# Kernel optimization log

Hardware: AMD Instinct MI355X
Metric: run time of the kernel (lower is better)

Reference implementation:

```python
import jax, jax.numpy as jnp
import numpy as np

NUM_HEADS = 16
BLOCK_SIZE = 64


def setup_inputs() -> dict:
    key = jax.random.key(0)
    ks = jax.random.split(key, 4)
    B, S, D = 4, 8192, 1024
    x = jax.random.normal(ks[0], (B, S, D), dtype=jnp.float32)
    Wq = jax.random.normal(ks[1], (D, D), dtype=jnp.float32) * 0.02
    Wk = jax.random.normal(ks[2], (D, D), dtype=jnp.float32) * 0.02
    Wv = jax.random.normal(ks[3], (D, D), dtype=jnp.float32) * 0.02
    bq = jnp.zeros((D,), dtype=jnp.float32)
    bk = jnp.zeros((D,), dtype=jnp.float32)
    bv = jnp.zeros((D,), dtype=jnp.float32)
    return {"x": x, "Wq": Wq, "bq": bq, "Wk": Wk, "bk": bk, "Wv": Wv, "bv": bv}


def reference(x, Wq, bq, Wk, bk, Wv, bv):
    # Block-diagonal local self-attention: token i attends only to tokens in
    # its own block [i//bs*bs, (i//bs+1)*bs). Equivalent to the original dense
    # mask, but computed block-wise (never materializing the SxS score matrix).
    B, S, D = x.shape
    H, bs = NUM_HEADS, BLOCK_SIZE
    d = D // H
    nb = S // bs

    q = (x @ Wq + bq).reshape(B, nb, bs, H, d)
    k = (x @ Wk + bk).reshape(B, nb, bs, H, d)
    v = (x @ Wv + bv).reshape(B, nb, bs, H, d)

    scale = 1.0 / jnp.sqrt(jnp.asarray(d, dtype=x.dtype))
    # per-block scores: [B, nb, H, bs, bs]
    scores = jnp.einsum("bnihd,bnjhd->bnhij", q, k) * scale
    attn = jax.nn.softmax(scores, axis=-1)
    out = jnp.einsum("bnhij,bnjhd->bnihd", attn, v)  # [B, nb, bs, H, d]
    return out.reshape(B, S, D)
```

## Files before the change

### kernel.cpp

```cpp
#include <hip/hip_runtime.h>
#include <hip/hip_bf16.h>

typedef __attribute__((ext_vector_type(8))) short short8;
typedef __attribute__((ext_vector_type(4))) float f32x4;
typedef unsigned short u16;

#define DIM     1024
#define NHEAD   16
#define HDIM    64
#define AS1 __attribute__((address_space(1)))
#define AS3 __attribute__((address_space(3)))

__device__ __forceinline__ u16 f2b(float f) {
  union { float f; unsigned u; } v; v.f = f;
  unsigned r = (v.u + 0x7FFFu + ((v.u >> 16) & 1u)) >> 16;
  return (u16)r;
}

__global__ void cvt_x_kernel(const float* __restrict__ in, u16* __restrict__ out, int n8) {
  int i = blockIdx.x * 256 + threadIdx.x;
  if (i >= n8) return;
  const float4* p = (const float4*)in + (size_t)i * 2;
  float4 a = p[0], c = p[1];
  short8 o;
  o[0] = (short)f2b(a.x); o[1] = (short)f2b(a.y); o[2] = (short)f2b(a.z); o[3] = (short)f2b(a.w);
  o[4] = (short)f2b(c.x); o[5] = (short)f2b(c.y); o[6] = (short)f2b(c.z); o[7] = (short)f2b(c.w);
  *((short8*)out + i) = o;
}

__global__ void cvt_wT_kernel(const float* __restrict__ Wq, const float* __restrict__ Wk,
                              const float* __restrict__ Wv, u16* __restrict__ wT) {
  int t = blockIdx.x * 256 + threadIdx.x;
  int mat = t >> 17;
  int rem = t & 131071;
  int kg  = rem >> 10;
  int n   = rem & 1023;
  const float* W = (mat == 0) ? Wq : (mat == 1) ? Wk : Wv;
  short8 v;
  #pragma unroll
  for (int i = 0; i < 8; ++i) v[i] = (short)f2b(W[(size_t)(kg * 8 + i) * DIM + n]);
  *(short8*)(wT + ((size_t)mat << 20) + (size_t)n * DIM + kg * 8) = v;
}

#define STAGE(matB, h, ktile) do { \
  const u16* _s = (matB) ? srcB : srcA; \
  _Pragma("unroll") \
  for (int _j = 0; _j < 2; ++_j) { \
    int _c = _j * 8 + wid; \
    __builtin_amdgcn_global_load_lds( \
      (const AS1 void*)(_s + (size_t)((h) * 128 + _c * 8) * DIM + (ktile) * 64), \
      (AS3 void*)(lds + ((((ktile) & 1) << 15) + ((matB) << 14) + ((h) << 13) + _c * 512)), \
      16, 0, 0); \
  } \
} while (0)

#define LDA(d, g) do { \
  _Pragma("unroll") \
  for (int _mi = 0; _mi < 4; ++_mi) { \
    int _r = abase + ((g) * 4 + _mi) * 1024 + ((d) << 15); \
    a[_mi * 2]     = *(const short8*)(lds + _r + sx0); \
    a[_mi * 2 + 1] = *(const short8*)(lds + _r + sx1); \
  } \
} while (0)

#define LDB(d, dst, nB) do { \
  _Pragma("unroll") \
  for (int _ni = 0; _ni < 2; ++_ni) { \
    int _r = bbase + ((nB) + _ni) * 1024 + ((d) << 15) + 16384; \
    dst[_ni * 2]     = *(const short8*)(lds + _r + sx0); \
    dst[_ni * 2 + 1] = *(const short8*)(lds + _r + sx1); \
  } \
} while (0)

#define MF(g, nB, bset) do { \
  _Pragma("unroll") \
  for (int _mi = 0; _mi < 4; ++_mi) \
    _Pragma("unroll") \
    for (int _ni = 0; _ni < 2; ++_ni) \
      _Pragma("unroll") \
      for (int _kk = 0; _kk < 2; ++_kk) \
        acc[(g) * 4 + _mi][(nB) + _ni] = __builtin_amdgcn_mfma_f32_16x16x32_bf16( \
            a[_mi * 2 + _kk], bset[_ni * 2 + _kk], acc[(g) * 4 + _mi][(nB) + _ni], 0, 0, 0); \
} while (0)

#define PH_MID() do { \
  __builtin_amdgcn_s_barrier(); \
  asm volatile("s_waitcnt lgkmcnt(0)" ::: "memory"); \
  __builtin_amdgcn_sched_barrier(0); \
  __builtin_amdgcn_s_setprio(1); \
} while (0)

#define PH_END() do { \
  __builtin_amdgcn_s_setprio(0); \
  __builtin_amdgcn_s_barrier(); \
} while (0)

#define PH_END_VM(n) do { \
  __builtin_amdgcn_s_setprio(0); \
  asm volatile("s_waitcnt vmcnt(" #n ")" ::: "memory"); \
  __builtin_amdgcn_s_barrier(); \
} while (0)

__global__ __launch_bounds__(512, 2) void qkv_gemm_kernel(
    const u16* __restrict__ xb, const u16* __restrict__ wT,
    const float* __restrict__ bq, const float* __restrict__ bk, const float* __restrict__ bv,
    u16* __restrict__ qb, u16* __restrict__ kb, u16* __restrict__ vb)
{
  __shared__ u16 lds[65536];

  const int tid  = threadIdx.x;
  const int lane = tid & 63;
  const int wid  = tid >> 6;

  const int orig = blockIdx.x;
  const int wg   = (orig & 7) * 192 + (orig >> 3);
  const int bm   = wg / 12;
  const int bn   = wg % 12;
  const int mat  = bn >> 2;
  const int col0 = (bn & 3) << 8;
  const int row0 = bm << 8;
  const u16* Wm = wT + ((size_t)mat << 20);
  const float* bias = (mat == 0) ? bq : (mat == 1) ? bk : bv;
  u16* outp = (mat == 0) ? qb : (mat == 1) ? kb : vb;

  const int wr = wid >> 2;
  const int wc = wid & 3;
  const int l15 = lane & 15, lhi = lane >> 4;

  const int sr = lane >> 3;
  const int sl = (lane & 7) ^ sr;
  const u16* srcA = xb + (size_t)(row0 + sr) * DIM + sl * 8;
  const u16* srcB = Wm + (size_t)(col0 + sr) * DIM + sl * 8;

  const int sx0 = (lhi ^ (l15 & 7)) << 3;
  const int sx1 = ((4 + lhi) ^ (l15 & 7)) << 3;
  const int abase = (wr * 128 + l15) * 64;
  const int bbase = (wc * 64 + l15) * 64;

  f32x4 acc[8][4] = {};
  short8 a[8], b01[4], b23[4];

  STAGE(0, 0, 0); STAGE(0, 1, 0); STAGE(1, 0, 0); STAGE(1, 1, 0);
  STAGE(0, 0, 1); STAGE(0, 1, 1);
  asm volatile("s_waitcnt vmcnt(4)" ::: "memory");
  __builtin_amdgcn_s_barrier();

  #pragma unroll 1
  for (int t = 0; t < 8; ++t) {
    const int kt = 2 * t;
    const bool pf = (t < 7);
    LDA(0, 0); LDB(0, b01, 0);
    STAGE(1, 0, kt + 1);
    asm volatile("s_waitcnt lgkmcnt(8)" ::: "memory");
    PH_MID(); MF(0, 0, b01); PH_END();
    LDB(0, b23, 2);
    STAGE(1, 1, kt + 1);
    PH_MID(); MF(0, 2, b23); PH_END();
    LDA(0, 1);
    PH_MID(); MF(1, 2, b23); PH_END();
    if (pf) STAGE(0, 0, kt + 2);
    PH_MID(); MF(1, 0, b01);
    if (pf) { PH_END_VM(2); } else { PH_END_VM(0); }
    LDA(1, 0); LDB(1, b01, 0);
    if (pf) STAGE(0, 1, kt + 2);
    asm volatile("s_waitcnt lgkmcnt(8)" ::: "memory");
    PH_MID(); MF(0, 0, b01); PH_END();
    LDB(1, b23, 2);
    if (pf) STAGE(1, 0, kt + 2);
    PH_MID(); MF(0, 2, b23); PH_END();
    LDA(1, 1);
    if (pf) STAGE(1, 1, kt + 2);
    PH_MID(); MF(1, 2, b23); PH_END();
    if (pf) { STAGE(0, 0, kt + 3); STAGE(0, 1, kt + 3); }
    PH_MID(); MF(1, 0, b01);
    if (pf) { PH_END_VM(4); } else { PH_END_VM(0); }
  }

  #pragma unroll
  for (int ni = 0; ni < 4; ++ni) {
    int gcol = col0 + wc * 64 + ni * 16 + l15;
    float bb = bias[gcol];
    #pragma unroll
    for (int mi = 0; mi < 8; ++mi) {
      int grow = row0 + wr * 128 + mi * 16 + (lhi << 2);
      #pragma unroll
      for (int r = 0; r < 4; ++r)
        outp[(size_t)(grow + r) * DIM + gcol] = f2b(acc[mi][ni][r] + bb);
    }
  }
}

__global__ __launch_bounds__(256) void blk_attn_kernel(
    const u16* __restrict__ qb, const u16* __restrict__ kb, const u16* __restrict__ vb,
    float* __restrict__ out)
{
  __shared__ u16 qs[64 * 72];
  __shared__ u16 ks[64 * 72];
  __shared__ u16 vts[64 * 72];
  __shared__ u16 ps[64 * 72];

  const int tid  = threadIdx.x;
  const int lane = tid & 63;
  const int wid  = tid >> 6;
  const int idx  = blockIdx.x;
  const int h    = idx & 15;
  const int blk  = (idx >> 4) & 127;
  const int b    = idx >> 11;
  const size_t s0 = (size_t)b * 8192 + (size_t)blk * 64;
  const int h0 = h * HDIM;

  {
    int i  = tid >> 2;
    int cg = (tid & 3) * 16;
    const u16* qg = qb + (s0 + i) * DIM + h0 + cg;
    *(short8*)(qs + i * 72 + cg)     = *(const short8*)qg;
    *(short8*)(qs + i * 72 + cg + 8) = *(const short8*)(qg + 8);
    const u16* kg = kb + (s0 + i) * DIM + h0 + cg;
    *(short8*)(ks + i * 72 + cg)     = *(const short8*)kg;
    *(short8*)(ks + i * 72 + cg + 8) = *(const short8*)(kg + 8);
    const u16* vg = vb + (s0 + i) * DIM + h0 + cg;
    short8 v0 = *(const short8*)vg;
    short8 v1 = *(const short8*)(vg + 8);
    #pragma unroll
    for (int e = 0; e < 8; ++e) {
      vts[(cg + e) * 72 + i]     = (u16)v0[e];
      vts[(cg + 8 + e) * 72 + i] = (u16)v1[e];
    }
  }
  __syncthreads();

  f32x4 S[4] = {};
  {
    short8 aq[2];
    #pragma unroll
    for (int kk = 0; kk < 2; ++kk)
      aq[kk] = *(const short8*)(qs + (wid * 16 + (lane & 15)) * 72 + kk * 32 + ((lane >> 4) << 3));
    #pragma unroll
    for (int jt = 0; jt < 4; ++jt)
      #pragma unroll
      for (int kk = 0; kk < 2; ++kk) {
        short8 bk_ = *(const short8*)(ks + (jt * 16 + (lane & 15)) * 72 + kk * 32 + ((lane >> 4) << 3));
        S[jt] = __builtin_amdgcn_mfma_f32_16x16x32_bf16(aq[kk], bk_, S[jt], 0, 0, 0);
      }
  }

  const float scale = 0.125f;
  float rinv[4];
  #pragma unroll
  for (int r = 0; r < 4; ++r) {
    float m = S[0][r] * scale;
    #pragma unroll
    for (int jt = 1; jt < 4; ++jt) m = fmaxf(m, S[jt][r] * scale);
    #pragma unroll
    for (int off = 1; off < 16; off <<= 1) m = fmaxf(m, __shfl_xor(m, off, 64));
    float s = 0.f;
    #pragma unroll
    for (int jt = 0; jt < 4; ++jt) {
      float e = __expf(S[jt][r] * scale - m);
      S[jt][r] = e;
      s += e;
    }
    #pragma unroll
    for (int off = 1; off < 16; off <<= 1) s += __shfl_xor(s, off, 64);
    rinv[r] = 1.0f / s;
  }

  #pragma unroll
  for (int jt = 0; jt < 4; ++jt)
    #pragma unroll
    for (int r = 0; r < 4; ++r)
      ps[(wid * 16 + ((lane >> 4) << 2) + r) * 72 + jt * 16 + (lane & 15)] = f2b(S[jt][r]);
  __syncthreads();

  f32x4 O[4] = {};
  {
    short8 pa[2];
    #pragma unroll
    for (int kk = 0; kk < 2; ++kk)
      pa[kk] = *(const short8*)(ps + (wid * 16 + (lane & 15)) * 72 + kk * 32 + ((lane >> 4) << 3));
    #pragma unroll
    for (int dt = 0; dt < 4; ++dt)
      #pragma unroll
      for (int kk = 0; kk < 2; ++kk) {
        short8 bv_ = *(const short8*)(vts + (dt * 16 + (lane & 15)) * 72 + kk * 32 + ((lane >> 4) << 3));
        O[dt] = __builtin_amdgcn_mfma_f32_16x16x32_bf16(pa[kk], bv_, O[dt], 0, 0, 0);
      }
  }

  #pragma unroll
  for (int dt = 0; dt < 4; ++dt)
    #pragma unroll
    for (int r = 0; r < 4; ++r)
      out[(s0 + wid * 16 + ((lane >> 4) << 2) + r) * DIM + h0 + dt * 16 + (lane & 15)] = O[dt][r] * rinv[r];
}

extern "C" void kernel_launch(void* const* d_in, const int* in_sizes, int n_in,
                              void* d_out, int out_size, void* d_ws, size_t ws_size,
                              hipStream_t stream) {
  const float* x  = (const float*)d_in[0];
  const float* Wq = (const float*)d_in[1];
  const float* bq = (const float*)d_in[2];
  const float* Wk = (const float*)d_in[3];
  const float* bk = (const float*)d_in[4];
  const float* Wv = (const float*)d_in[5];
  const float* bv = (const float*)d_in[6];
  float* out = (float*)d_out;

  char* ws = (char*)d_ws;
  u16* xb = (u16*)ws;
  u16* wT = (u16*)(ws + 67108864);
  u16* qb = (u16*)(ws + 73400320);
  u16* kb = (u16*)(ws + 140509184);
  u16* vb = (u16*)(ws + 207618048);

  cvt_x_kernel<<<16384, 256, 0, stream>>>(x, xb, 4194304);
  cvt_wT_kernel<<<1536, 256, 0, stream>>>(Wq, Wk, Wv, wT);
  qkv_gemm_kernel<<<1536, 512, 0, stream>>>(xb, wT, bq, bk, bv, qb, kb, vb);
  blk_attn_kernel<<<8192, 256, 0, stream>>>(qb, kb, vb, out);
}
```

Baseline: 345.0 us.

## Restructure QKV GEMM prefetch into quadrant-ordered stages with finer vmcnt waits

```diff
diff --git a/kernel.cpp b/kernel.cpp
--- a/kernel.cpp
+++ b/kernel.cpp
@@ -42,14 +42,18 @@
   *(short8*)(wT + ((size_t)mat << 20) + (size_t)n * DIM + kg * 8) = v;
 }
 
-#define STAGE(matB, h, ktile) do { \
-  const u16* _s = (matB) ? srcB : srcA; \
+#define VMW_(n) asm volatile("s_waitcnt vmcnt(" #n ")" ::: "memory")
+#define VMW(n) VMW_(n)
+
+#define STAGE_P(isB, isOdd, ktile) do { \
   _Pragma("unroll") \
   for (int _j = 0; _j < 2; ++_j) { \
-    int _c = _j * 8 + wid; \
+    int _b = _j * 8 + wid; \
+    int _r0 = (isB) ? (((_b >> 2) << 6) + ((_b & 3) << 3) + ((isOdd) << 5)) \
+                    : (((_b >> 3) << 7) + ((_b & 7) << 3) + ((isOdd) << 6)); \
     __builtin_amdgcn_global_load_lds( \
-      (const AS1 void*)(_s + (size_t)((h) * 128 + _c * 8) * DIM + (ktile) * 64), \
-      (AS3 void*)(lds + ((((ktile) & 1) << 15) + ((matB) << 14) + ((h) << 13) + _c * 512)), \
+      (const AS1 void*)(((isB) ? srcB : srcA) + (size_t)_r0 * DIM + (ktile) * 64), \
+      (AS3 void*)(lds + ((((ktile) & 1) << 15) + ((isB) << 14) + _r0 * 64)), \
       16, 0, 0); \
   } \
 } while (0)
@@ -90,15 +94,26 @@
   __builtin_amdgcn_s_setprio(1); \
 } while (0)
 
-#define PH_END() do { \
-  __builtin_amdgcn_s_setprio(0); \
-  __builtin_amdgcn_s_barrier(); \
-} while (0)
-
-#define PH_END_VM(n) do { \
-  __builtin_amdgcn_s_setprio(0); \
-  asm volatile("s_waitcnt vmcnt(" #n ")" ::: "memory"); \
-  __builtin_amdgcn_s_barrier(); \
+#define GROUP(d, j2, DOST, G1n, G2n, G4n) do { \
+   \
+  LDA(d, 0); LDB(d, b01, 0); \
+  asm volatile("s_waitcnt lgkmcnt(8)" ::: "memory"); \
+  PH_MID(); MF(0, 0, b01); \
+  __builtin_amdgcn_s_setprio(0); VMW(G1n); __builtin_amdgcn_s_barrier(); \
+   \
+  LDB(d, b23, 2); \
+  if (DOST) { STAGE_P(0, 0, j2); STAGE_P(1, 0, j2); } \
+  PH_MID(); MF(0, 2, b23); \
+  __builtin_amdgcn_s_setprio(0); VMW(G2n); __builtin_amdgcn_s_barrier(); \
+   \
+  LDA(d, 1); \
+  if (DOST) STAGE_P(1, 1, j2); \
+  PH_MID(); MF(1, 2, b23); \
+  __builtin_amdgcn_s_setprio(0); __builtin_amdgcn_s_barrier(); \
+   \
+  if (DOST) STAGE_P(0, 1, j2); \
+  PH_MID(); MF(1, 0, b01); \
+  __builtin_amdgcn_s_setprio(0); VMW(G4n); __builtin_amdgcn_s_barrier(); \
 } while (0)
 
 __global__ __launch_bounds__(512, 2) void qkv_gemm_kernel(
@@ -140,41 +155,18 @@
   f32x4 acc[8][4] = {};
   short8 a[8], b01[4], b23[4];
 
-  STAGE(0, 0, 0); STAGE(0, 1, 0); STAGE(1, 0, 0); STAGE(1, 1, 0);
-  STAGE(0, 0, 1); STAGE(0, 1, 1);
-  asm volatile("s_waitcnt vmcnt(4)" ::: "memory");
+  STAGE_P(0, 0, 0); STAGE_P(1, 0, 0); STAGE_P(1, 1, 0); STAGE_P(0, 1, 0);
+  STAGE_P(0, 0, 1); STAGE_P(1, 0, 1); STAGE_P(1, 1, 1); STAGE_P(0, 1, 1);
+  VMW(8);
   __builtin_amdgcn_s_barrier();
 
   #pragma unroll 1
-  for (int t = 0; t < 8; ++t) {
-    const int kt = 2 * t;
-    const bool pf = (t < 7);
-    LDA(0, 0); LDB(0, b01, 0);
-    STAGE(1, 0, kt + 1);
-    asm volatile("s_waitcnt lgkmcnt(8)" ::: "memory");
-    PH_MID(); MF(0, 0, b01); PH_END();
-    LDB(0, b23, 2);
-    STAGE(1, 1, kt + 1);
-    PH_MID(); MF(0, 2, b23); PH_END();
-    LDA(0, 1);
-    PH_MID(); MF(1, 2, b23); PH_END();
-    if (pf) STAGE(0, 0, kt + 2);
-    PH_MID(); MF(1, 0, b01);
-    if (pf) { PH_END_VM(2); } else { PH_END_VM(0); }
-    LDA(1, 0); LDB(1, b01, 0);
-    if (pf) STAGE(0, 1, kt + 2);
-    asm volatile("s_waitcnt lgkmcnt(8)" ::: "memory");
-    PH_MID(); MF(0, 0, b01); PH_END();
-    LDB(1, b23, 2);
-    if (pf) STAGE(1, 0, kt + 2);
-    PH_MID(); MF(0, 2, b23); PH_END();
-    LDA(1, 1);
-    if (pf) STAGE(1, 1, kt + 2);
-    PH_MID(); MF(1, 2, b23); PH_END();
-    if (pf) { STAGE(0, 0, kt + 3); STAGE(0, 1, kt + 3); }
-    PH_MID(); MF(1, 0, b01);
-    if (pf) { PH_END_VM(4); } else { PH_END_VM(0); }
-  }
+  for (int t = 0; t < 7; ++t) {
+    GROUP(0, 2 * t + 2, 1, 10, 12, 12);
+    GROUP(1, 2 * t + 3, 1, 10, 12, 12);
+  }
+  GROUP(0, 16, 0, 10, 8, 4);
+  GROUP(1, 17, 0, 2, 0, 0);
 
   #pragma unroll
   for (int ni = 0; ni < 4; ++ni) {
```

After: 396.4 us. 14.9% more time.
